# Optimization experiments

Hardware: AMD Instinct MI355X
Metric: run time of the kernel (lower is better)

Reference implementation:

```python
import jax, jax.numpy as jnp
import numpy as np

IN_F = 256
OUT_F = 256
ALPHA = 0.2  # leaky-relu slope
NEG_INF = -9e15


def setup_inputs() -> dict:
    key = jax.random.key(0)
    ks = jax.random.split(key, 8)
    N_e, N_kc = 10000, 2000
    exercise_h = jax.random.normal(ks[0], (N_e, IN_F), dtype=jnp.float32)
    kc_h = jax.random.normal(ks[1], (N_kc, IN_F), dtype=jnp.float32)
    adj = jax.random.randint(ks[2], (N_e, N_kc), 0, 2, dtype=jnp.int32)
    # parameters (kaiming-ish scaling)
    W1 = jax.random.normal(ks[3], (IN_F, OUT_F), dtype=jnp.float32) * np.sqrt(2.0 / IN_F)
    E = jax.random.normal(ks[4], (IN_F, OUT_F), dtype=jnp.float32) * np.sqrt(2.0 / IN_F)
    a = jax.random.normal(ks[5], (2 * OUT_F, 1), dtype=jnp.float32) * np.sqrt(2.0 / (2 * OUT_F))
    rd_w = jax.random.normal(ks[6], (OUT_F, 2 * OUT_F), dtype=jnp.float32) * np.sqrt(2.0 / (2 * OUT_F))
    rd_b = jnp.zeros((OUT_F,), dtype=jnp.float32)
    return {"exercise_h": exercise_h, "kc_h": kc_h, "adj": adj,
            "W1": W1, "E": E, "a": a, "rd_w": rd_w, "rd_b": rd_b}


def reference(exercise_h, kc_h, adj, W1, E, a, rd_w, rd_b):
    kc_Wh = kc_h @ W1            # [N_kc, D]
    ex_Wh = exercise_h @ W1      # [N_e, D]
    # a . concat(ex_Wh_i, kc_Wh_j) == a1.ex_Wh_i + a2.kc_Wh_j  (avoids [N_e,N_kc,2D] tensor)
    a1 = a[:OUT_F, 0]
    a2 = a[OUT_F:, 0]
    e = jax.nn.leaky_relu((ex_Wh @ a1)[:, None] + (kc_Wh @ a2)[None, :], negative_slope=ALPHA)  # [N_e, N_kc]
    logits = jnp.where(adj > 0, e, jnp.float32(NEG_INF))
    attention = jax.nn.softmax(logits, axis=1)
    new_kc = attention @ kc_Wh           # [N_e, D]
    ex_Eh = exercise_h @ E               # [N_e, D]
    feat = jnp.concatenate([new_kc, new_kc * ex_Eh], axis=1)  # [N_e, 2D]
    out = feat @ rd_w.T + rd_b
    return jax.nn.elu(out)
```

## Files before the change

kernel.cpp:

```cpp
#include <hip/hip_runtime.h>

#define N_E 10000
#define N_KC 2000
#define ALPHA 0.2f

typedef __attribute__((ext_vector_type(8))) short short8;
typedef __attribute__((ext_vector_type(4))) float f32x4;

__device__ float g_w1a1[256];
__device__ float g_t[2048];
__device__ __align__(16) unsigned short g_W1T_pk[16 * 8 * 512];
__device__ __align__(16) unsigned short g_ET_pk[16 * 8 * 512];
__device__ __align__(16) unsigned short g_rdw_pk[16 * 16 * 512];
__device__ __align__(16) unsigned short g_kcWh_pk[16 * 64 * 512];

__device__ __forceinline__ unsigned short f2bf(float f) {
  union { float f; unsigned int u; } v; v.f = f;
  unsigned int r = v.u + 0x7FFFu + ((v.u >> 16) & 1u);
  return (unsigned short)(r >> 16);
}

__device__ __forceinline__ void cvt_store4(float4 v, unsigned short* dst) {
  ushort4 o;
  o.x = f2bf(v.x); o.y = f2bf(v.y); o.z = f2bf(v.z); o.w = f2bf(v.w);
  *reinterpret_cast<ushort4*>(dst) = o;
}

__global__ __launch_bounds__(256) void prep_kernel(
    const float* __restrict__ W1, const float* __restrict__ E,
    const float* __restrict__ a, const float* __restrict__ rd_w) {
  int b = blockIdx.x, tid = threadIdx.x;
  if (b < 32) {
#pragma unroll
    for (int s2 = 0; s2 < 2; ++s2) {
      int sId = b * 512 + tid + s2 * 256;
      int ct = sId >> 10, rem = sId & 1023;
      int kt = rem >> 6, lane = rem & 63;
      int g = lane >> 4, r = lane & 15;
      const float* src = rd_w + (size_t)(ct * 16 + r) * 512 + kt * 32 + g * 8;
      unsigned short* dst = g_rdw_pk + (size_t)sId * 8;
      cvt_store4(*(const float4*)src, dst);
      cvt_store4(*(const float4*)(src + 4), dst + 4);
    }
  } else if (b < 48) {
#pragma unroll
    for (int s2 = 0; s2 < 2; ++s2) {
      int sId = (b - 32) * 512 + tid + s2 * 256;
      int ct = sId >> 9, rem = sId & 511;
      int kt = rem >> 6, lane = rem & 63;
      int g = lane >> 4, r = lane & 15;
      int col = ct * 16 + r, k = kt * 32 + g * 8;
      unsigned short* dst = g_W1T_pk + (size_t)sId * 8;
      ushort4 o0, o1;
      o0.x = f2bf(W1[(k + 0) * 256 + col]); o0.y = f2bf(W1[(k + 1) * 256 + col]);
      o0.z = f2bf(W1[(k + 2) * 256 + col]); o0.w = f2bf(W1[(k + 3) * 256 + col]);
      o1.x = f2bf(W1[(k + 4) * 256 + col]); o1.y = f2bf(W1[(k + 5) * 256 + col]);
      o1.z = f2bf(W1[(k + 6) * 256 + col]); o1.w = f2bf(W1[(k + 7) * 256 + col]);
      *(ushort4*)dst = o0; *(ushort4*)(dst + 4) = o1;
    }
  } else if (b < 64) {
#pragma unroll
    for (int s2 = 0; s2 < 2; ++s2) {
      int sId = (b - 48) * 512 + tid + s2 * 256;
      int ct = sId >> 9, rem = sId & 511;
      int kt = rem >> 6, lane = rem & 63;
      int g = lane >> 4, r = lane & 15;
      int col = ct * 16 + r, k = kt * 32 + g * 8;
      unsigned short* dst = g_ET_pk + (size_t)sId * 8;
      ushort4 o0, o1;
      o0.x = f2bf(E[(k + 0) * 256 + col]); o0.y = f2bf(E[(k + 1) * 256 + col]);
      o0.z = f2bf(E[(k + 2) * 256 + col]); o0.w = f2bf(E[(k + 3) * 256 + col]);
      o1.x = f2bf(E[(k + 4) * 256 + col]); o1.y = f2bf(E[(k + 5) * 256 + col]);
      o1.z = f2bf(E[(k + 6) * 256 + col]); o1.w = f2bf(E[(k + 7) * 256 + col]);
      *(ushort4*)dst = o0; *(ushort4*)(dst + 4) = o1;
    }
  } else if (b == 64) {
    float acc = 0.f;
    for (int q = 0; q < 64; ++q) {
      float4 wv = *(const float4*)(W1 + (size_t)tid * 256 + q * 4);
      float4 a4 = *(const float4*)(a + q * 4);
      acc += wv.x * a4.x + wv.y * a4.y + wv.z * a4.z + wv.w * a4.w;
    }
    g_w1a1[tid] = acc;
  } else {
    for (int idx = tid; idx < 16 * 2 * 512; idx += 256) {
      int ct = idx >> 10, rem = idx & 1023;
      int kt = 62 + (rem >> 9), off = rem & 511;
      g_kcWh_pk[((size_t)ct * 64 + kt) * 512 + off] = 0;
    }
    if (tid < 48) g_t[2000 + tid] = 0.f;
  }
}

__global__ __launch_bounds__(256) void kc_mfma_kernel(
    const float* __restrict__ kc_h, const float* __restrict__ a) {
  __shared__ float tred[4][4][4];
  int tid = threadIdx.x, lane = tid & 63, w = tid >> 6;
  int r = lane & 15, g = lane >> 4;
  int j0 = blockIdx.x * 16;
  f32x4 acc[4] = {{0.f,0.f,0.f,0.f},{0.f,0.f,0.f,0.f},
                  {0.f,0.f,0.f,0.f},{0.f,0.f,0.f,0.f}};
  for (int kk = 0; kk < 8; ++kk) {
    int k = kk * 32 + g * 8;
    const float* src = kc_h + (size_t)(j0 + r) * 256 + k;
    float4 x0 = *(const float4*)src, x1 = *(const float4*)(src + 4);
    short8 af = {(short)f2bf(x0.x), (short)f2bf(x0.y), (short)f2bf(x0.z),
                 (short)f2bf(x0.w), (short)f2bf(x1.x), (short)f2bf(x1.y),
                 (short)f2bf(x1.z), (short)f2bf(x1.w)};
#pragma unroll
    for (int n = 0; n < 4; ++n) {
      short8 bf = *(const short8*)(g_W1T_pk + ((size_t)(w * 4 + n) * 8 + kk) *
                                                  512 + lane * 8);
      acc[n] = __builtin_amdgcn_mfma_f32_16x16x32_bf16(af, bf, acc[n], 0, 0, 0);
    }
  }
  int j = j0 + g * 4;
  int kt = j >> 5, lsub = ((j >> 3) & 3) * 16 + r, sub = (g & 1) * 4;
#pragma unroll
  for (int n = 0; n < 4; ++n) {
    int ct = w * 4 + n;
    ushort4 o;
    o.x = f2bf(acc[n][0]); o.y = f2bf(acc[n][1]);
    o.z = f2bf(acc[n][2]); o.w = f2bf(acc[n][3]);
    *reinterpret_cast<ushort4*>(
        g_kcWh_pk + ((size_t)ct * 64 + kt) * 512 + lsub * 8 + sub) = o;
  }
  float a2v[4];
#pragma unroll
  for (int n = 0; n < 4; ++n) a2v[n] = a[256 + w * 64 + n * 16 + r];
  float tp[4];
#pragma unroll
  for (int q = 0; q < 4; ++q)
    tp[q] = acc[0][q] * a2v[0] + acc[1][q] * a2v[1] + acc[2][q] * a2v[2] +
            acc[3][q] * a2v[3];
#pragma unroll
  for (int off = 1; off < 16; off <<= 1)
#pragma unroll
    for (int q = 0; q < 4; ++q) tp[q] += __shfl_xor(tp[q], off, 64);
  if (r == 0)
#pragma unroll
    for (int q = 0; q < 4; ++q) tred[w][g][q] = tp[q];
  __syncthreads();
  if (tid < 16)
    g_t[j0 + tid] = tred[0][tid >> 2][tid & 3] + tred[1][tid >> 2][tid & 3] +
                    tred[2][tid >> 2][tid & 3] + tred[3][tid >> 2][tid & 3];
}

#define PSTR 136
#define FST 536
__global__ __launch_bounds__(512, 4) void main_kernel(
    const float* __restrict__ exh, const int* __restrict__ adj,
    const float* __restrict__ rd_b, float* __restrict__ out) {
  __shared__ __align__(16) unsigned char smem[41984];
  __shared__ float ds_part[8][32];
  __shared__ float red32[32];
  float* t_s = (float*)smem;
  unsigned short* p_s = (unsigned short*)(smem + 8192);
  unsigned short* exh_pk_s = (unsigned short*)(smem + 25600);
  unsigned short* feat_s = (unsigned short*)smem;

  int tid = threadIdx.x, w = tid >> 6, lane = tid & 63;
  int r = lane & 15, g = lane >> 4;
  int i0 = blockIdx.x * 32;
  int mh = w >> 2;
  int kw = w & 3;

  ((float4*)t_s)[tid] = ((const float4*)g_t)[tid];
  {
    const float* wsrc = g_w1a1 + w * 32 + g * 8;
    float4 w0 = *(const float4*)wsrc, w1 = *(const float4*)(wsrc + 4);
    float sp[2];
#pragma unroll
    for (int m = 0; m < 2; ++m) {
      int row = i0 + m * 16 + r; row = row < N_E ? row : N_E - 1;
      const float* xsrc = exh + (size_t)row * 256 + w * 32 + g * 8;
      float4 x0 = *(const float4*)xsrc, x1 = *(const float4*)(xsrc + 4);
      unsigned short* dst = exh_pk_s + m * 4096 + w * 512 + lane * 8;
      cvt_store4(x0, dst); cvt_store4(x1, dst + 4);
      sp[m] = x0.x * w0.x + x0.y * w0.y + x0.z * w0.z + x0.w * w0.w +
              x1.x * w1.x + x1.y * w1.y + x1.z * w1.z + x1.w * w1.w;
      sp[m] += __shfl_xor(sp[m], 16, 64);
      sp[m] += __shfl_xor(sp[m], 32, 64);
    }
    if (lane < 16) { ds_part[w][lane] = sp[0]; ds_part[w][16 + lane] = sp[1]; }
  }
  __syncthreads();
  if (tid < 32) {
    float sv = 0.f;
#pragma unroll
    for (int ww = 0; ww < 8; ++ww) sv += ds_part[ww][tid];
    red32[tid] = sv;
  }
  __syncthreads();
  float sv = red32[mh * 16 + r];
  int grow = i0 + mh * 16 + r; grow = grow < N_E ? grow : N_E - 1;
  const int* arow = adj + (size_t)grow * N_KC;

  f32x4 accP[2][2] = {{{0.f,0.f,0.f,0.f},{0.f,0.f,0.f,0.f}},
                      {{0.f,0.f,0.f,0.f},{0.f,0.f,0.f,0.f}}};
  float dsum = 0.f;

  auto gen = [&](int c) {
    int kk = c * 4 + kw;
    int c0 = kk * 32 + g * 8;
    int4 pk = {0, 0, 0, 0};
    if (kk < 63 && c0 < N_KC) {
      int4 a0 = *(const int4*)(arow + c0);
      int4 a1 = *(const int4*)(arow + c0 + 4);
      float4 t0 = *(const float4*)(t_s + c0);
      float4 t1 = *(const float4*)(t_s + c0 + 4);
      float tv[8] = {t0.x, t0.y, t0.z, t0.w, t1.x, t1.y, t1.z, t1.w};
      int av[8] = {a0.x, a0.y, a0.z, a0.w, a1.x, a1.y, a1.z, a1.w};
      unsigned ub[8];
#pragma unroll
      for (int j = 0; j < 8; ++j) {
        float x = sv + tv[j];
        float lx = fmaxf(x, ALPHA * x);
        float pv = (av[j] > 0) ? __expf(lx) : 0.f;
        dsum += pv;
        ub[j] = __float_as_uint(pv) + 0x8000u;
      }
      pk.x = (int)((ub[0] >> 16) | (ub[1] & 0xFFFF0000u));
      pk.y = (int)((ub[2] >> 16) | (ub[3] & 0xFFFF0000u));
      pk.z = (int)((ub[4] >> 16) | (ub[5] & 0xFFFF0000u));
      pk.w = (int)((ub[6] >> 16) | (ub[7] & 0xFFFF0000u));
    }
    *(int4*)(p_s + ((size_t)(c & 1) * 32 + mh * 16 + r) * PSTR + kw * 32 +
             g * 8) = pk;
  };

  auto mfma_chunk = [&](int c) {
    const unsigned short* pb = p_s + (size_t)(c & 1) * 32 * PSTR;
    const unsigned short* bb0 =
        g_kcWh_pk + ((size_t)(w * 2 + 0) * 64 + c * 4) * 512 + lane * 8;
    const unsigned short* bb1 =
        g_kcWh_pk + ((size_t)(w * 2 + 1) * 64 + c * 4) * 512 + lane * 8;
    short8 b0 = *(const short8*)bb0;
    short8 b1 = *(const short8*)bb1;
#pragma unroll
    for (int u = 0; u < 4; ++u) {
      short8 a0 = *(const short8*)(pb + (size_t)r * PSTR + u * 32 + g * 8);
      short8 a1 = *(const short8*)(pb + (size_t)(16 + r) * PSTR + u * 32 + g * 8);
      short8 nb0 = b0, nb1 = b1;
      if (u < 3) {
        nb0 = *(const short8*)(bb0 + (u + 1) * 512);
        nb1 = *(const short8*)(bb1 + (u + 1) * 512);
      }
      accP[0][0] = __builtin_amdgcn_mfma_f32_16x16x32_bf16(a0, b0, accP[0][0], 0, 0, 0);
      accP[1][0] = __builtin_amdgcn_mfma_f32_16x16x32_bf16(a1, b0, accP[1][0], 0, 0, 0);
      accP[0][1] = __builtin_amdgcn_mfma_f32_16x16x32_bf16(a0, b1, accP[0][1], 0, 0, 0);
      accP[1][1] = __builtin_amdgcn_mfma_f32_16x16x32_bf16(a1, b1, accP[1][1], 0, 0, 0);
      b0 = nb0; b1 = nb1;
    }
  };

  gen(0);
  __syncthreads();
  for (int c = 1; c < 16; ++c) {
    gen(c);
    mfma_chunk(c - 1);
    __syncthreads();
  }
  mfma_chunk(15);

  dsum += __shfl_xor(dsum, 16, 64);
  dsum += __shfl_xor(dsum, 32, 64);
  if (lane < 16) {
    ds_part[w][mh * 16 + lane] = dsum;
    ds_part[w][(1 - mh) * 16 + lane] = 0.f;
  }

  f32x4 accE[2][2] = {{{0.f,0.f,0.f,0.f},{0.f,0.f,0.f,0.f}},
                      {{0.f,0.f,0.f,0.f},{0.f,0.f,0.f,0.f}}};
#pragma unroll
  for (int kk = 0; kk < 8; ++kk) {
    short8 a0 = *(const short8*)(exh_pk_s + kk * 512 + lane * 8);
    short8 a1 = *(const short8*)(exh_pk_s + 4096 + kk * 512 + lane * 8);
#pragma unroll
    for (int n = 0; n < 2; ++n) {
      short8 bf = *(const short8*)(g_ET_pk + ((size_t)(w * 2 + n) * 8 + kk) *
                                                 512 + lane * 8);
      accE[0][n] = __builtin_amdgcn_mfma_f32_16x16x32_bf16(a0, bf, accE[0][n], 0, 0, 0);
      accE[1][n] = __builtin_amdgcn_mfma_f32_16x16x32_bf16(a1, bf, accE[1][n], 0, 0, 0);
    }
  }
  __syncthreads();
  if (tid < 32) {
    float s = 0.f;
#pragma unroll
    for (int ww = 0; ww < 8; ++ww) s += ds_part[ww][tid];
    red32[tid] = 1.f / fmaxf(s, 1e-30f);
  }
  __syncthreads();

  int c0e = w * 32;
#pragma unroll
  for (int m = 0; m < 2; ++m)
#pragma unroll
    for (int n = 0; n < 2; ++n) {
      int col = c0e + n * 16 + r;
#pragma unroll
      for (int q = 0; q < 4; ++q) {
        int row = m * 16 + g * 4 + q;
        float nk = accP[m][n][q] * red32[row];
        feat_s[(size_t)row * FST + col] = f2bf(nk);
        feat_s[(size_t)row * FST + 256 + col] = f2bf(nk * accE[m][n][q]);
      }
    }
  __syncthreads();

  f32x4 accO[2][2] = {{{0.f,0.f,0.f,0.f},{0.f,0.f,0.f,0.f}},
                      {{0.f,0.f,0.f,0.f},{0.f,0.f,0.f,0.f}}};
#pragma unroll
  for (int kt = 0; kt < 16; ++kt) {
    int k = kt * 32 + g * 8;
    short8 a0 = *(const short8*)(feat_s + (size_t)r * FST + k);
    short8 a1 = *(const short8*)(feat_s + (size_t)(16 + r) * FST + k);
#pragma unroll
    for (int n = 0; n < 2; ++n) {
      short8 bf = *(const short8*)(g_rdw_pk + ((size_t)(w * 2 + n) * 16 + kt) *
                                                  512 + lane * 8);
      accO[0][n] = __builtin_amdgcn_mfma_f32_16x16x32_bf16(a0, bf, accO[0][n], 0, 0, 0);
      accO[1][n] = __builtin_amdgcn_mfma_f32_16x16x32_bf16(a1, bf, accO[1][n], 0, 0, 0);
    }
  }
#pragma unroll
  for (int m = 0; m < 2; ++m) {
    if (i0 + m * 16 >= N_E) continue;
#pragma unroll
    for (int n = 0; n < 2; ++n) {
      int col = c0e + n * 16 + r;
      float bias = rd_b[col];
#pragma unroll
      for (int q = 0; q < 4; ++q) {
        int row = i0 + m * 16 + g * 4 + q;
        float x = accO[m][n][q] + bias;
        float res = x > 0.f ? x : (__expf(x) - 1.f);
        out[(size_t)row * 256 + col] = res;
      }
    }
  }
}

extern "C" void kernel_launch(void* const* d_in, const int* in_sizes, int n_in,
                              void* d_out, int out_size, void* d_ws,
                              size_t ws_size, hipStream_t stream) {
  const float* exh  = (const float*)d_in[0];
  const float* kc_h = (const float*)d_in[1];
  const int*   adj  = (const int*)d_in[2];
  const float* W1   = (const float*)d_in[3];
  const float* E    = (const float*)d_in[4];
  const float* a    = (const float*)d_in[5];
  const float* rd_w = (const float*)d_in[6];
  const float* rd_b = (const float*)d_in[7];
  float* out = (float*)d_out;

  prep_kernel<<<66, 256, 0, stream>>>(W1, E, a, rd_w);
  kc_mfma_kernel<<<N_KC / 16, 256, 0, stream>>>(kc_h, a);
  main_kernel<<<(N_E + 31) / 32, 512, 0, stream>>>(exh, adj, rd_b, out);
}
```

Baseline: 183.9 us.

## Precompute adjacency bitmask, split kc projection across blocks, interleave E-projection MFMAs

A new stage in the prep kernel compresses the int32 adjacency matrix into a per-row 64-bit bitmask using wave ballots. The main kernel then reads compact bitmasks into shared memory instead of streaming int32 adjacency inside the softmax generation loop. The kc projection kernel is split four ways across column tiles and accumulates the attention scalar with atomics, which gives more blocks. The ex·E MFMAs are interleaved into the attention chunk loop to overlap them. The adjacency still has to be read in full once, by the prep kernel, and the prep grid grows to thousands of blocks.

```diff
diff --git a/kernel.cpp b/kernel.cpp
--- a/kernel.cpp
+++ b/kernel.cpp
@@ -8,7 +8,8 @@
 typedef __attribute__((ext_vector_type(4))) float f32x4;
 
 __device__ float g_w1a1[256];
-__device__ float g_t[2048];
+__device__ __align__(16) float g_t[2080];
+__device__ unsigned long long g_bm64[N_E * 32];
 __device__ __align__(16) unsigned short g_W1T_pk[16 * 8 * 512];
 __device__ __align__(16) unsigned short g_ET_pk[16 * 8 * 512];
 __device__ __align__(16) unsigned short g_rdw_pk[16 * 16 * 512];
@@ -26,9 +27,19 @@
   *reinterpret_cast<ushort4*>(dst) = o;
 }
 
+__device__ __forceinline__ unsigned long long spread4(unsigned long long x) {
+  x &= 0xFFFFull;
+  x = (x | (x << 24)) & 0x000000FF000000FFull;
+  x = (x | (x << 12)) & 0x000F000F000F000Full;
+  x = (x | (x << 6))  & 0x0303030303030303ull;
+  x = (x | (x << 3))  & 0x1111111111111111ull;
+  return x;
+}
+
 __global__ __launch_bounds__(256) void prep_kernel(
-    const float* __restrict__ W1, const float* __restrict__ E,
-    const float* __restrict__ a, const float* __restrict__ rd_w) {
+    const int* __restrict__ adj, const float* __restrict__ W1,
+    const float* __restrict__ E, const float* __restrict__ a,
+    const float* __restrict__ rd_w) {
   int b = blockIdx.x, tid = threadIdx.x;
   if (b < 32) {
 #pragma unroll
@@ -82,24 +93,43 @@
       acc += wv.x * a4.x + wv.y * a4.y + wv.z * a4.z + wv.w * a4.w;
     }
     g_w1a1[tid] = acc;
-  } else {
+  } else if (b == 65) {
     for (int idx = tid; idx < 16 * 2 * 512; idx += 256) {
       int ct = idx >> 10, rem = idx & 1023;
       int kt = 62 + (rem >> 9), off = rem & 511;
       g_kcWh_pk[((size_t)ct * 64 + kt) * 512 + off] = 0;
     }
-    if (tid < 48) g_t[2000 + tid] = 0.f;
+    for (int idx = tid; idx < 2080; idx += 256) g_t[idx] = 0.f;
+  } else {
+    int w = tid >> 6, lane = tid & 63;
+    int row = (b - 66) * 4 + w;
+    const int* ap = adj + (size_t)row * N_KC;
+#pragma unroll
+    for (int it = 0; it < 8; ++it) {
+      int c0 = it * 256 + lane * 4;
+      int4 v = {0, 0, 0, 0};
+      if (c0 < N_KC) v = *(const int4*)(ap + c0);
+      unsigned long long m0 = __ballot(v.x > 0);
+      unsigned long long m1 = __ballot(v.y > 0);
+      unsigned long long m2 = __ballot(v.z > 0);
+      unsigned long long m3 = __ballot(v.w > 0);
+      if (lane < 4) {
+        int sh = lane * 16;
+        unsigned long long W = spread4(m0 >> sh) | (spread4(m1 >> sh) << 1) |
+                               (spread4(m2 >> sh) << 2) | (spread4(m3 >> sh) << 3);
+        g_bm64[(size_t)row * 32 + it * 4 + lane] = W;
+      }
+    }
   }
 }
 
 __global__ __launch_bounds__(256) void kc_mfma_kernel(
     const float* __restrict__ kc_h, const float* __restrict__ a) {
-  __shared__ float tred[4][4][4];
   int tid = threadIdx.x, lane = tid & 63, w = tid >> 6;
   int r = lane & 15, g = lane >> 4;
-  int j0 = blockIdx.x * 16;
-  f32x4 acc[4] = {{0.f,0.f,0.f,0.f},{0.f,0.f,0.f,0.f},
-                  {0.f,0.f,0.f,0.f},{0.f,0.f,0.f,0.f}};
+  int j0 = (blockIdx.x >> 2) * 16;
+  int ct = (blockIdx.x & 3) * 4 + w;
+  f32x4 acc = {0.f, 0.f, 0.f, 0.f};
   for (int kk = 0; kk < 8; ++kk) {
     int k = kk * 32 + g * 8;
     const float* src = kc_h + (size_t)(j0 + r) * 256 + k;
@@ -107,65 +137,55 @@
     short8 af = {(short)f2bf(x0.x), (short)f2bf(x0.y), (short)f2bf(x0.z),
                  (short)f2bf(x0.w), (short)f2bf(x1.x), (short)f2bf(x1.y),
                  (short)f2bf(x1.z), (short)f2bf(x1.w)};
-#pragma unroll
-    for (int n = 0; n < 4; ++n) {
-      short8 bf = *(const short8*)(g_W1T_pk + ((size_t)(w * 4 + n) * 8 + kk) *
-                                                  512 + lane * 8);
-      acc[n] = __builtin_amdgcn_mfma_f32_16x16x32_bf16(af, bf, acc[n], 0, 0, 0);
-    }
+    short8 bf = *(const short8*)(g_W1T_pk + ((size_t)ct * 8 + kk) * 512 +
+                                 lane * 8);
+    acc = __builtin_amdgcn_mfma_f32_16x16x32_bf16(af, bf, acc, 0, 0, 0);
   }
   int j = j0 + g * 4;
   int kt = j >> 5, lsub = ((j >> 3) & 3) * 16 + r, sub = (g & 1) * 4;
-#pragma unroll
-  for (int n = 0; n < 4; ++n) {
-    int ct = w * 4 + n;
-    ushort4 o;
-    o.x = f2bf(acc[n][0]); o.y = f2bf(acc[n][1]);
-    o.z = f2bf(acc[n][2]); o.w = f2bf(acc[n][3]);
-    *reinterpret_cast<ushort4*>(
-        g_kcWh_pk + ((size_t)ct * 64 + kt) * 512 + lsub * 8 + sub) = o;
-  }
-  float a2v[4];
-#pragma unroll
-  for (int n = 0; n < 4; ++n) a2v[n] = a[256 + w * 64 + n * 16 + r];
+  ushort4 o;
+  o.x = f2bf(acc[0]); o.y = f2bf(acc[1]); o.z = f2bf(acc[2]); o.w = f2bf(acc[3]);
+  *reinterpret_cast<ushort4*>(
+      g_kcWh_pk + ((size_t)ct * 64 + kt) * 512 + lsub * 8 + sub) = o;
+  float a2v = a[256 + ct * 16 + r];
   float tp[4];
 #pragma unroll
-  for (int q = 0; q < 4; ++q)
-    tp[q] = acc[0][q] * a2v[0] + acc[1][q] * a2v[1] + acc[2][q] * a2v[2] +
-            acc[3][q] * a2v[3];
+  for (int q = 0; q < 4; ++q) tp[q] = acc[q] * a2v;
 #pragma unroll
   for (int off = 1; off < 16; off <<= 1)
 #pragma unroll
     for (int q = 0; q < 4; ++q) tp[q] += __shfl_xor(tp[q], off, 64);
   if (r == 0)
 #pragma unroll
-    for (int q = 0; q < 4; ++q) tred[w][g][q] = tp[q];
-  __syncthreads();
-  if (tid < 16)
-    g_t[j0 + tid] = tred[0][tid >> 2][tid & 3] + tred[1][tid >> 2][tid & 3] +
-                    tred[2][tid >> 2][tid & 3] + tred[3][tid >> 2][tid & 3];
+    for (int q = 0; q < 4; ++q) atomicAdd(&g_t[j0 + g * 4 + q], tp[q]);
 }
 
 #define PSTR 136
 #define FST 536
 __global__ __launch_bounds__(512, 4) void main_kernel(
-    const float* __restrict__ exh, const int* __restrict__ adj,
-    const float* __restrict__ rd_b, float* __restrict__ out) {
-  __shared__ __align__(16) unsigned char smem[41984];
+    const float* __restrict__ exh, const float* __restrict__ rd_b,
+    float* __restrict__ out) {
+  __shared__ __align__(16) unsigned char smem[50816];
   __shared__ float ds_part[8][32];
   __shared__ float red32[32];
   float* t_s = (float*)smem;
-  unsigned short* p_s = (unsigned short*)(smem + 8192);
-  unsigned short* exh_pk_s = (unsigned short*)(smem + 25600);
+  unsigned long long* bm_s = (unsigned long long*)(smem + 8320);
+  unsigned short* p_s = (unsigned short*)(smem + 17024);
+  unsigned short* exh_pk_s = (unsigned short*)(smem + 34432);
   unsigned short* feat_s = (unsigned short*)smem;
 
   int tid = threadIdx.x, w = tid >> 6, lane = tid & 63;
   int r = lane & 15, g = lane >> 4;
   int i0 = blockIdx.x * 32;
-  int mh = w >> 2;
-  int kw = w & 3;
-
-  ((float4*)t_s)[tid] = ((const float4*)g_t)[tid];
+  int mh = w >> 2, kw = w & 3;
+
+  for (int q = tid; q < 520; q += 512)
+    ((float4*)t_s)[q] = ((const float4*)g_t)[q];
+  for (int q = tid; q < 32 * 32; q += 512) {
+    int rr = q >> 5, wd = q & 31;
+    int grow = i0 + rr; grow = grow < N_E ? grow : N_E - 1;
+    bm_s[rr * 34 + wd] = g_bm64[(size_t)grow * 32 + wd];
+  }
   {
     const float* wsrc = g_w1a1 + w * 32 + g * 8;
     float4 w0 = *(const float4*)wsrc, w1 = *(const float4*)(wsrc + 4);
@@ -193,38 +213,35 @@
   }
   __syncthreads();
   float sv = red32[mh * 16 + r];
-  int grow = i0 + mh * 16 + r; grow = grow < N_E ? grow : N_E - 1;
-  const int* arow = adj + (size_t)grow * N_KC;
 
   f32x4 accP[2][2] = {{{0.f,0.f,0.f,0.f},{0.f,0.f,0.f,0.f}},
+                      {{0.f,0.f,0.f,0.f},{0.f,0.f,0.f,0.f}}};
+  f32x4 accE[2][2] = {{{0.f,0.f,0.f,0.f},{0.f,0.f,0.f,0.f}},
                       {{0.f,0.f,0.f,0.f},{0.f,0.f,0.f,0.f}}};
   float dsum = 0.f;
 
   auto gen = [&](int c) {
     int kk = c * 4 + kw;
     int c0 = kk * 32 + g * 8;
-    int4 pk = {0, 0, 0, 0};
-    if (kk < 63 && c0 < N_KC) {
-      int4 a0 = *(const int4*)(arow + c0);
-      int4 a1 = *(const int4*)(arow + c0 + 4);
-      float4 t0 = *(const float4*)(t_s + c0);
-      float4 t1 = *(const float4*)(t_s + c0 + 4);
-      float tv[8] = {t0.x, t0.y, t0.z, t0.w, t1.x, t1.y, t1.z, t1.w};
-      int av[8] = {a0.x, a0.y, a0.z, a0.w, a1.x, a1.y, a1.z, a1.w};
-      unsigned ub[8];
-#pragma unroll
-      for (int j = 0; j < 8; ++j) {
-        float x = sv + tv[j];
-        float lx = fmaxf(x, ALPHA * x);
-        float pv = (av[j] > 0) ? __expf(lx) : 0.f;
-        dsum += pv;
-        ub[j] = __float_as_uint(pv) + 0x8000u;
-      }
-      pk.x = (int)((ub[0] >> 16) | (ub[1] & 0xFFFF0000u));
-      pk.y = (int)((ub[2] >> 16) | (ub[3] & 0xFFFF0000u));
-      pk.z = (int)((ub[4] >> 16) | (ub[5] & 0xFFFF0000u));
-      pk.w = (int)((ub[6] >> 16) | (ub[7] & 0xFFFF0000u));
-    }
+    unsigned mb =
+        (unsigned)((bm_s[(mh * 16 + r) * 34 + (c0 >> 6)] >> (c0 & 63)) & 0xFFull);
+    float4 t0 = *(const float4*)(t_s + c0);
+    float4 t1 = *(const float4*)(t_s + c0 + 4);
+    float tv[8] = {t0.x, t0.y, t0.z, t0.w, t1.x, t1.y, t1.z, t1.w};
+    unsigned ub[8];
+#pragma unroll
+    for (int j = 0; j < 8; ++j) {
+      float x = sv + tv[j];
+      float lx = fmaxf(x, ALPHA * x);
+      float pv = ((mb >> j) & 1u) ? __expf(lx) : 0.f;
+      dsum += pv;
+      ub[j] = __float_as_uint(pv) + 0x8000u;
+    }
+    int4 pk;
+    pk.x = (int)((ub[0] >> 16) | (ub[1] & 0xFFFF0000u));
+    pk.y = (int)((ub[2] >> 16) | (ub[3] & 0xFFFF0000u));
+    pk.z = (int)((ub[4] >> 16) | (ub[5] & 0xFFFF0000u));
+    pk.w = (int)((ub[6] >> 16) | (ub[7] & 0xFFFF0000u));
     *(int4*)(p_s + ((size_t)(c & 1) * 32 + mh * 16 + r) * PSTR + kw * 32 +
              g * 8) = pk;
   };
@@ -252,6 +269,18 @@
       accP[1][1] = __builtin_amdgcn_mfma_f32_16x16x32_bf16(a1, b1, accP[1][1], 0, 0, 0);
       b0 = nb0; b1 = nb1;
     }
+    if ((c & 1) == 0) {
+      int ke = c >> 1;
+      short8 a0 = *(const short8*)(exh_pk_s + ke * 512 + lane * 8);
+      short8 a1 = *(const short8*)(exh_pk_s + 4096 + ke * 512 + lane * 8);
+#pragma unroll
+      for (int n = 0; n < 2; ++n) {
+        short8 be = *(const short8*)(g_ET_pk + ((size_t)(w * 2 + n) * 8 + ke) *
+                                                   512 + lane * 8);
+        accE[0][n] = __builtin_amdgcn_mfma_f32_16x16x32_bf16(a0, be, accE[0][n], 0, 0, 0);
+        accE[1][n] = __builtin_amdgcn_mfma_f32_16x16x32_bf16(a1, be, accE[1][n], 0, 0, 0);
+      }
+    }
   };
 
   gen(0);
@@ -268,21 +297,6 @@
   if (lane < 16) {
     ds_part[w][mh * 16 + lane] = dsum;
     ds_part[w][(1 - mh) * 16 + lane] = 0.f;
-  }
-
-  f32x4 accE[2][2] = {{{0.f,0.f,0.f,0.f},{0.f,0.f,0.f,0.f}},
-                      {{0.f,0.f,0.f,0.f},{0.f,0.f,0.f,0.f}}};
-#pragma unroll
-  for (int kk = 0; kk < 8; ++kk) {
-    short8 a0 = *(const short8*)(exh_pk_s + kk * 512 + lane * 8);
-    short8 a1 = *(const short8*)(exh_pk_s + 4096 + kk * 512 + lane * 8);
-#pragma unroll
-    for (int n = 0; n < 2; ++n) {
-      short8 bf = *(const short8*)(g_ET_pk + ((size_t)(w * 2 + n) * 8 + kk) *
-                                                 512 + lane * 8);
-      accE[0][n] = __builtin_amdgcn_mfma_f32_16x16x32_bf16(a0, bf, accE[0][n], 0, 0, 0);
-      accE[1][n] = __builtin_amdgcn_mfma_f32_16x16x32_bf16(a1, bf, accE[1][n], 0, 0, 0);
-    }
   }
   __syncthreads();
   if (tid < 32) {
@@ -355,7 +369,7 @@
   const float* rd_b = (const float*)d_in[7];
   float* out = (float*)d_out;
 
-  prep_kernel<<<66, 256, 0, stream>>>(W1, E, a, rd_w);
-  kc_mfma_kernel<<<N_KC / 16, 256, 0, stream>>>(kc_h, a);
-  main_kernel<<<(N_E + 31) / 32, 512, 0, stream>>>(exh, adj, rd_b, out);
-}
+  prep_kernel<<<2566, 256, 0, stream>>>(adj, W1, E, a, rd_w);
+  kc_mfma_kernel<<<500, 256, 0, stream>>>(kc_h, a);
+  main_kernel<<<(N_E + 31) / 32, 512, 0, stream>>>(exh, rd_b, out);
+}
```

Measured after the change: 187.3 us. About the same (+1.9%).
